# Kernel tuning notes

Measured on AMD Instinct MI355X. Metric: run time of the kernel, lower is better.

## Reference

```python
import jax, jax.numpy as jnp
import numpy as np

MARGIN = 1.0
N, D = 4096, 512
NUM_CLASSES = 64


def setup_inputs() -> dict:
    key = jax.random.key(0)
    k1, k2 = jax.random.split(key)
    inputs = jax.random.normal(k1, (N, D), dtype=jnp.float32)
    targets = jax.random.randint(k2, (N,), 0, NUM_CLASSES, dtype=jnp.int64)
    return {"inputs": inputs, "targets": targets}


def reference(inputs, targets):
    n = inputs.shape[0]
    sq = jnp.sum(inputs * inputs, axis=1)  # [n]
    # squared Euclidean distances, clamped at 0 (matches relu in original)
    d2 = jnp.maximum(sq[:, None] + sq[None, :] - 2.0 * (inputs @ inputs.T), 0.0)
    # safe sqrt (zero entries get 0, matching forward; avoids NaN grads)
    dist = jnp.where(d2 > 0, jnp.sqrt(jnp.where(d2 > 0, d2, 1.0)), 0.0)  # [n,n]

    same = targets[:, None] == targets[None, :]
    eye = jnp.eye(n, dtype=bool)
    pos_mask = same & ~eye          # positives, diagonal excluded
    neg_mask = ~same                # negatives (diagonal is same-label, excluded)

    # per-row sum_k exp(margin - d_ik) over negatives  (replaces per-pair loop)
    neg_sum = jnp.sum(jnp.where(neg_mask, jnp.exp(MARGIN - dist), 0.0), axis=1)  # [n]

    # J_ij = log(neg_sum_i + neg_sum_j) + d_ij for positive pairs
    J = jnp.log(neg_sum[:, None] + neg_sum[None, :]) + dist
    triu_pos = jnp.triu(pos_mask)   # loop iterated over upper-triangular positives
    hinge2 = jnp.where(triu_pos, jax.nn.relu(J) ** 2, 0.0)

    # original divides by count of ALL positive entries (both triangles)
    len_p = jnp.sum(pos_mask).astype(jnp.float32)
    return jnp.sum(hinge2) / len_p
```

## Files before the change

kernel.cpp:

```cpp
#include <hip/hip_runtime.h>
#include <math.h>

#define NN 4096
#define DD 512
#define MARGINF 1.0f
#define NCLS 64
#define MAXM 160
#define TRI (MAXM * (MAXM - 1) / 2)
#define NBLK 2080

typedef __attribute__((ext_vector_type(8))) short bf16x8;
typedef __attribute__((ext_vector_type(4))) float f32x4;

#define WS_SQ   0
#define WS_NS   4096
#define WS_LOSS 8192
#define WS_CTR  8193
#define WS_CNT  8256
#define WS_RK   8320
#define WS_MEM  12416
#define WS_XF   32768
#define WS_PD   1081344

__device__ __forceinline__ unsigned short f2bf(float f) {
    unsigned u = __float_as_uint(f);
    u += 0x7fffu + ((u >> 16) & 1u);
    return (unsigned short)(u >> 16);
}

__global__ __launch_bounds__(256) void prep_kernel(const float* __restrict__ X,
                                                   float* __restrict__ ws) {
    const int wv = threadIdx.x >> 6, lane = threadIdx.x & 63;
    const int row = blockIdx.x * 4 + wv;
    const float4* xr = (const float4*)(X + (size_t)row * DD);
    float4 a = xr[2 * lane], b = xr[2 * lane + 1];
    float s = a.x * a.x + a.y * a.y + a.z * a.z + a.w * a.w
            + b.x * b.x + b.y * b.y + b.z * b.z + b.w * b.w;
#pragma unroll
    for (int off = 32; off; off >>= 1) s += __shfl_down(s, off, 64);
    if (lane == 0) { ws[WS_SQ + row] = s; ws[WS_NS + row] = 0.0f; }
    ushort4 pa = {f2bf(a.x), f2bf(a.y), f2bf(a.z), f2bf(a.w)};
    ushort4 pb = {f2bf(b.x), f2bf(b.y), f2bf(b.z), f2bf(b.w)};
    const int r16 = row >> 4, m = row & 15;
    const int kb = lane >> 2, q = lane & 3;
    ushort4* dst = (ushort4*)((unsigned short*)(ws + WS_XF)
                              + ((size_t)(r16 * 16 + kb) * 64 + q * 16 + m) * 8);
    dst[0] = pa;
    dst[1] = pb;
    if (blockIdx.x == 0) {
        if (threadIdx.x < NCLS) ((int*)(ws + WS_CNT))[threadIdx.x] = 0;
        if (threadIdx.x == 0) { ws[WS_LOSS] = 0.0f; ((unsigned*)ws)[WS_CTR] = 0u; }
    }
}

__global__ __launch_bounds__(256) void class_build_kernel(const int* __restrict__ tgt,
                                                          float* __restrict__ ws) {
    const int t = blockIdx.x * 256 + threadIdx.x;
    const int c = tgt[t];
    int p = atomicAdd(&((int*)(ws + WS_CNT))[c], 1);
    ((int*)(ws + WS_RK))[t] = p;
    if (p < MAXM) ((int*)(ws + WS_MEM))[c * MAXM + p] = t;
}

__global__ __launch_bounds__(256, 6) void negsum_kernel(const int* __restrict__ tgt,
                                                        float* __restrict__ ws) {
    const int bidx = blockIdx.x;
    int bj = (int)((sqrtf(8.0f * (float)bidx + 1.0f) - 1.0f) * 0.5f);
    while (bj * (bj + 1) / 2 > bidx) --bj;
    while ((bj + 1) * (bj + 2) / 2 <= bidx) ++bj;
    const int bi = bidx - bj * (bj + 1) / 2;
    const int i0 = bi * 64, j0 = bj * 64;

    const int tid = threadIdx.x;
    const int w = tid >> 6, lane = tid & 63;
    const int m_ = lane & 15, q = lane >> 4;
    const int wr = (w & 1) * 32, wc = (w >> 1) * 32;
    const unsigned short* Xf = (const unsigned short*)(ws + WS_XF);

    const int air = (i0 + wr) >> 4;
    const int bjr = (j0 + wc) >> 4;
    const unsigned short* pA = Xf + (size_t)air * 8192 + lane * 8;
    const unsigned short* pB = Xf + (size_t)bjr * 8192 + lane * 8;

    f32x4 acc[2][2] = {};
    bf16x8 af[2], bfr[2], nA[2], nB[2];
#pragma unroll
    for (int u = 0; u < 2; ++u) {
        af[u]  = *(const bf16x8*)(pA + u * 8192);
        bfr[u] = *(const bf16x8*)(pB + u * 8192);
    }
#pragma unroll
    for (int it = 0; it < 16; ++it) {
        if (it < 15) {
#pragma unroll
            for (int u = 0; u < 2; ++u) {
                nA[u] = *(const bf16x8*)(pA + u * 8192 + (it + 1) * 512);
                nB[u] = *(const bf16x8*)(pB + u * 8192 + (it + 1) * 512);
            }
        }
        acc[0][0] = __builtin_amdgcn_mfma_f32_16x16x32_bf16(af[0], bfr[0], acc[0][0], 0, 0, 0);
        acc[0][1] = __builtin_amdgcn_mfma_f32_16x16x32_bf16(af[0], bfr[1], acc[0][1], 0, 0, 0);
        acc[1][0] = __builtin_amdgcn_mfma_f32_16x16x32_bf16(af[1], bfr[0], acc[1][0], 0, 0, 0);
        acc[1][1] = __builtin_amdgcn_mfma_f32_16x16x32_bf16(af[1], bfr[1], acc[1][1], 0, 0, 0);
#pragma unroll
        for (int u = 0; u < 2; ++u) { af[u] = nA[u]; bfr[u] = nB[u]; }
    }

    const float* sq = ws + WS_SQ;
    float* ns = ws + WS_NS;
    const int* rk = (const int*)(ws + WS_RK);
    float* posd = ws + WS_PD;
    float sjv[2]; int tjv[2], jv[2];
#pragma unroll
    for (int v = 0; v < 2; ++v) {
        int j = j0 + wc + v * 16 + m_;
        jv[v] = j;
        sjv[v] = sq[j];
        tjv[v] = tgt[j];
    }
    float colp[2] = {0.0f, 0.0f};
#pragma unroll
    for (int u = 0; u < 2; ++u) {
#pragma unroll
        for (int r = 0; r < 4; ++r) {
            const int i = i0 + wr + u * 16 + q * 4 + r;
            const float si = sq[i];
            const int ti = tgt[i];
            float rp = 0.0f;
#pragma unroll
            for (int v = 0; v < 2; ++v) {
                float d2 = si + sjv[v] - 2.0f * acc[u][v][r];
                float dist = d2 > 0.0f ? sqrtf(d2) : 0.0f;
                if (tjv[v] != ti) {
                    float e = __expf(MARGINF - dist);
                    rp += e;
                    colp[v] += e;
                } else if (i < jv[v]) {
                    int ra = rk[i], rb = rk[jv[v]];
                    if (ra < MAXM && rb < MAXM) {
                        int hi = ra > rb ? ra : rb;
                        int lo = ra > rb ? rb : ra;
                        posd[ti * TRI + hi * (hi - 1) / 2 + lo] = dist;
                    }
                }
            }
            rp += __shfl_xor(rp, 1, 64);
            rp += __shfl_xor(rp, 2, 64);
            rp += __shfl_xor(rp, 4, 64);
            rp += __shfl_xor(rp, 8, 64);
            if (m_ == 0) atomicAdd(&ns[i], rp);
        }
    }
    if (bi != bj) {
#pragma unroll
        for (int v = 0; v < 2; ++v) {
            float cp = colp[v];
            cp += __shfl_xor(cp, 16, 64);
            cp += __shfl_xor(cp, 32, 64);
            if (q == 0) atomicAdd(&ns[jv[v]], cp);
        }
    }
}

__global__ __launch_bounds__(256) void pair2_kernel(float* __restrict__ ws,
                                                    float* __restrict__ out) {
    __shared__ float wsum[4];
    __shared__ bool last;
    const int c = blockIdx.x;
    const int tid = threadIdx.x;
    int mc = ((const int*)(ws + WS_CNT))[c];
    if (mc > MAXM) mc = MAXM;
    const int P = mc * (mc - 1) / 2;
    const int* mem = (const int*)(ws + WS_MEM) + c * MAXM;
    const float* pd = ws + WS_PD + c * TRI;
    const float* ns = ws + WS_NS;
    float lsum = 0.0f;
    for (int p = tid; p < P; p += 256) {
        int b = (int)((1.0f + sqrtf(1.0f + 8.0f * (float)p)) * 0.5f);
        while (b * (b - 1) / 2 > p) --b;
        while ((b + 1) * b / 2 <= p) ++b;
        const int a = p - b * (b - 1) / 2;
        const float dist = pd[b * (b - 1) / 2 + a];
        const int i = mem[a], j = mem[b];
        float J = __logf(ns[i] + ns[j]) + dist;
        float h = fmaxf(J, 0.0f);
        lsum += h * h;
    }
#pragma unroll
    for (int off = 32; off; off >>= 1) lsum += __shfl_xor(lsum, off, 64);
    const int wv = tid >> 6, lane = tid & 63;
    if (lane == 0) wsum[wv] = lsum;
    __syncthreads();
    if (tid == 0) {
        float s = wsum[0] + wsum[1] + wsum[2] + wsum[3];
        if (s != 0.0f) atomicAdd(&ws[WS_LOSS], s);
        __threadfence();
        unsigned d = atomicAdd((unsigned*)ws + WS_CTR, 1u);
        last = (d == NCLS - 1);
    }
    __syncthreads();
    if (last && tid < 64) {
        int mcv = ((const int*)(ws + WS_CNT))[tid];
        float lp = (float)(mcv * (mcv - 1));
#pragma unroll
        for (int off = 32; off; off >>= 1) lp += __shfl_down(lp, off, 64);
        if (tid == 0) {
            float total = atomicAdd(&ws[WS_LOSS], 0.0f);
            out[0] = total / lp;
        }
    }
}

extern "C" void kernel_launch(void* const* d_in, const int* in_sizes, int n_in,
                              void* d_out, int out_size, void* d_ws, size_t ws_size,
                              hipStream_t stream) {
    const float* X  = (const float*)d_in[0];
    const int*  tgt = (const int*)d_in[1];
    float* ws  = (float*)d_ws;
    float* out = (float*)d_out;

    hipLaunchKernelGGL(prep_kernel, dim3(NN / 4), dim3(256), 0, stream, X, ws);
    hipLaunchKernelGGL(class_build_kernel, dim3(NN / 256), dim3(256), 0, stream, tgt, ws);
    hipLaunchKernelGGL(negsum_kernel, dim3(NBLK), dim3(256), 0, stream, tgt, ws);
    hipLaunchKernelGGL(pair2_kernel, dim3(NCLS), dim3(256), 0, stream, ws, out);
}
```

Measured before the change: 120.4 us.

## Fold class membership build into prep kernel and deepen MFMA prefetch

Drops the separate class_build launch. Each row's in-class rank is now computed deterministically in prep_kernel by counting earlier rows with the same label, using a shared-memory copy of the targets. pair2 recounts class sizes from the targets and accumulates the positive-pair count atomically, so the count-array initialisation is no longer needed. negsum switches to a three-stage register prefetch ring with launch bounds lowered to 5 waves. The cost is redundant O(N) label scans in every prep block and every pair2 block.

```diff
diff --git a/kernel.cpp b/kernel.cpp
--- a/kernel.cpp
+++ b/kernel.cpp
@@ -16,7 +16,7 @@
 #define WS_NS   4096
 #define WS_LOSS 8192
 #define WS_CTR  8193
-#define WS_CNT  8256
+#define WS_LENP 8194
 #define WS_RK   8320
 #define WS_MEM  12416
 #define WS_XF   32768
@@ -29,8 +29,13 @@
 }
 
 __global__ __launch_bounds__(256) void prep_kernel(const float* __restrict__ X,
+                                                   const int* __restrict__ tgt,
                                                    float* __restrict__ ws) {
-    const int wv = threadIdx.x >> 6, lane = threadIdx.x & 63;
+    __shared__ int tg[NN];
+    const int tid = threadIdx.x;
+    for (int j = tid; j < NN; j += 256) tg[j] = tgt[j];
+
+    const int wv = tid >> 6, lane = tid & 63;
     const int row = blockIdx.x * 4 + wv;
     const float4* xr = (const float4*)(X + (size_t)row * DD);
     float4 a = xr[2 * lane], b = xr[2 * lane + 1];
@@ -38,7 +43,7 @@
             + b.x * b.x + b.y * b.y + b.z * b.z + b.w * b.w;
 #pragma unroll
     for (int off = 32; off; off >>= 1) s += __shfl_down(s, off, 64);
-    if (lane == 0) { ws[WS_SQ + row] = s; ws[WS_NS + row] = 0.0f; }
+
     ushort4 pa = {f2bf(a.x), f2bf(a.y), f2bf(a.z), f2bf(a.w)};
     ushort4 pb = {f2bf(b.x), f2bf(b.y), f2bf(b.z), f2bf(b.w)};
     const int r16 = row >> 4, m = row & 15;
@@ -47,22 +52,27 @@
                               + ((size_t)(r16 * 16 + kb) * 64 + q * 16 + m) * 8);
     dst[0] = pa;
     dst[1] = pb;
-    if (blockIdx.x == 0) {
-        if (threadIdx.x < NCLS) ((int*)(ws + WS_CNT))[threadIdx.x] = 0;
-        if (threadIdx.x == 0) { ws[WS_LOSS] = 0.0f; ((unsigned*)ws)[WS_CTR] = 0u; }
-    }
-}
-
-__global__ __launch_bounds__(256) void class_build_kernel(const int* __restrict__ tgt,
-                                                          float* __restrict__ ws) {
-    const int t = blockIdx.x * 256 + threadIdx.x;
-    const int c = tgt[t];
-    int p = atomicAdd(&((int*)(ws + WS_CNT))[c], 1);
-    ((int*)(ws + WS_RK))[t] = p;
-    if (p < MAXM) ((int*)(ws + WS_MEM))[c * MAXM + p] = t;
-}
-
-__global__ __launch_bounds__(256, 6) void negsum_kernel(const int* __restrict__ tgt,
+
+    __syncthreads();
+    const int myc = tg[row];
+    int cnt = 0;
+    for (int j = lane; j < row; j += 64) cnt += (tg[j] == myc) ? 1 : 0;
+#pragma unroll
+    for (int off = 32; off; off >>= 1) cnt += __shfl_down(cnt, off, 64);
+    if (lane == 0) {
+        ws[WS_SQ + row] = s;
+        ws[WS_NS + row] = 0.0f;
+        ((int*)(ws + WS_RK))[row] = cnt;
+        if (cnt < MAXM) ((int*)(ws + WS_MEM))[myc * MAXM + cnt] = row;
+    }
+    if (blockIdx.x == 0 && tid == 0) {
+        ws[WS_LOSS] = 0.0f;
+        ((unsigned*)ws)[WS_CTR] = 0u;
+        ws[WS_LENP] = 0.0f;
+    }
+}
+
+__global__ __launch_bounds__(256, 5) void negsum_kernel(const int* __restrict__ tgt,
                                                         float* __restrict__ ws) {
     const int bidx = blockIdx.x;
     int bj = (int)((sqrtf(8.0f * (float)bidx + 1.0f) - 1.0f) * 0.5f);
@@ -83,27 +93,28 @@
     const unsigned short* pB = Xf + (size_t)bjr * 8192 + lane * 8;
 
     f32x4 acc[2][2] = {};
-    bf16x8 af[2], bfr[2], nA[2], nB[2];
-#pragma unroll
-    for (int u = 0; u < 2; ++u) {
-        af[u]  = *(const bf16x8*)(pA + u * 8192);
-        bfr[u] = *(const bf16x8*)(pB + u * 8192);
-    }
+    bf16x8 rgA[3][2], rgB[3][2];
+#pragma unroll
+    for (int s = 0; s < 2; ++s)
+#pragma unroll
+        for (int u = 0; u < 2; ++u) {
+            rgA[s][u] = *(const bf16x8*)(pA + u * 8192 + s * 512);
+            rgB[s][u] = *(const bf16x8*)(pB + u * 8192 + s * 512);
+        }
 #pragma unroll
     for (int it = 0; it < 16; ++it) {
-        if (it < 15) {
+        const int cur = it % 3, nx = (it + 2) % 3;
+        if (it < 14) {
 #pragma unroll
             for (int u = 0; u < 2; ++u) {
-                nA[u] = *(const bf16x8*)(pA + u * 8192 + (it + 1) * 512);
-                nB[u] = *(const bf16x8*)(pB + u * 8192 + (it + 1) * 512);
+                rgA[nx][u] = *(const bf16x8*)(pA + u * 8192 + (it + 2) * 512);
+                rgB[nx][u] = *(const bf16x8*)(pB + u * 8192 + (it + 2) * 512);
             }
         }
-        acc[0][0] = __builtin_amdgcn_mfma_f32_16x16x32_bf16(af[0], bfr[0], acc[0][0], 0, 0, 0);
-        acc[0][1] = __builtin_amdgcn_mfma_f32_16x16x32_bf16(af[0], bfr[1], acc[0][1], 0, 0, 0);
-        acc[1][0] = __builtin_amdgcn_mfma_f32_16x16x32_bf16(af[1], bfr[0], acc[1][0], 0, 0, 0);
-        acc[1][1] = __builtin_amdgcn_mfma_f32_16x16x32_bf16(af[1], bfr[1], acc[1][1], 0, 0, 0);
-#pragma unroll
-        for (int u = 0; u < 2; ++u) { af[u] = nA[u]; bfr[u] = nB[u]; }
+        acc[0][0] = __builtin_amdgcn_mfma_f32_16x16x32_bf16(rgA[cur][0], rgB[cur][0], acc[0][0], 0, 0, 0);
+        acc[0][1] = __builtin_amdgcn_mfma_f32_16x16x32_bf16(rgA[cur][0], rgB[cur][1], acc[0][1], 0, 0, 0);
+        acc[1][0] = __builtin_amdgcn_mfma_f32_16x16x32_bf16(rgA[cur][1], rgB[cur][0], acc[1][0], 0, 0, 0);
+        acc[1][1] = __builtin_amdgcn_mfma_f32_16x16x32_bf16(rgA[cur][1], rgB[cur][1], acc[1][1], 0, 0, 0);
     }
 
     const float* sq = ws + WS_SQ;
@@ -162,15 +173,26 @@
     }
 }
 
-__global__ __launch_bounds__(256) void pair2_kernel(float* __restrict__ ws,
+__global__ __launch_bounds__(256) void pair2_kernel(const int* __restrict__ tgt,
+                                                    float* __restrict__ ws,
                                                     float* __restrict__ out) {
     __shared__ float wsum[4];
+    __shared__ int csum[4];
     __shared__ bool last;
     const int c = blockIdx.x;
     const int tid = threadIdx.x;
-    int mc = ((const int*)(ws + WS_CNT))[c];
+    const int wv = tid >> 6, lane = tid & 63;
+
+    int ccount = 0;
+    for (int j = tid; j < NN; j += 256) ccount += (tgt[j] == c) ? 1 : 0;
+#pragma unroll
+    for (int off = 32; off; off >>= 1) ccount += __shfl_down(ccount, off, 64);
+    if (lane == 0) csum[wv] = ccount;
+    __syncthreads();
+    int mc = csum[0] + csum[1] + csum[2] + csum[3];
     if (mc > MAXM) mc = MAXM;
     const int P = mc * (mc - 1) / 2;
+
     const int* mem = (const int*)(ws + WS_MEM) + c * MAXM;
     const float* pd = ws + WS_PD + c * TRI;
     const float* ns = ws + WS_NS;
@@ -188,26 +210,21 @@
     }
 #pragma unroll
     for (int off = 32; off; off >>= 1) lsum += __shfl_xor(lsum, off, 64);
-    const int wv = tid >> 6, lane = tid & 63;
     if (lane == 0) wsum[wv] = lsum;
     __syncthreads();
     if (tid == 0) {
         float s = wsum[0] + wsum[1] + wsum[2] + wsum[3];
         if (s != 0.0f) atomicAdd(&ws[WS_LOSS], s);
+        atomicAdd(&ws[WS_LENP], (float)(mc * (mc - 1)));
         __threadfence();
         unsigned d = atomicAdd((unsigned*)ws + WS_CTR, 1u);
         last = (d == NCLS - 1);
     }
     __syncthreads();
-    if (last && tid < 64) {
-        int mcv = ((const int*)(ws + WS_CNT))[tid];
-        float lp = (float)(mcv * (mcv - 1));
-#pragma unroll
-        for (int off = 32; off; off >>= 1) lp += __shfl_down(lp, off, 64);
-        if (tid == 0) {
-            float total = atomicAdd(&ws[WS_LOSS], 0.0f);
-            out[0] = total / lp;
-        }
+    if (last && tid == 0) {
+        float total = atomicAdd(&ws[WS_LOSS], 0.0f);
+        float lp = atomicAdd(&ws[WS_LENP], 0.0f);
+        out[0] = total / lp;
     }
 }
 
@@ -219,8 +236,7 @@
     float* ws  = (float*)d_ws;
     float* out = (float*)d_out;
 
-    hipLaunchKernelGGL(prep_kernel, dim3(NN / 4), dim3(256), 0, stream, X, ws);
-    hipLaunchKernelGGL(class_build_kernel, dim3(NN / 256), dim3(256), 0, stream, tgt, ws);
+    hipLaunchKernelGGL(prep_kernel, dim3(NN / 4), dim3(256), 0, stream, X, tgt, ws);
     hipLaunchKernelGGL(negsum_kernel, dim3(NBLK), dim3(256), 0, stream, tgt, ws);
-    hipLaunchKernelGGL(pair2_kernel, dim3(NCLS), dim3(256), 0, stream, ws, out);
-}
+    hipLaunchKernelGGL(pair2_kernel, dim3(NCLS), dim3(256), 0, stream, tgt, ws, out);
+}
```

Result: faster. 116.8 us (-3.0%).
